# Kernel tuning notes

Hardware: AMD Instinct MI355X
Metric: run time of the kernel (lower is better)

The kernel has to match this reference:

```python
import jax, jax.numpy as jnp
import numpy as np

B, T, C, H = 2, 2048, 1024, 16
HD = C // H          # head_dim = 64
HALF = HD // 2       # rope half dim = 32
ROPE_BASE = 10000.0


def _build_sin_cos(seq_len, half_dim, base=ROPE_BASE):
    # mirrors build_sin_cos: angles[t, i] = t * base^(-2i / (2*half_dim))
    pos = jnp.arange(seq_len, dtype=jnp.float32)[:, None]                     # [T,1]
    inv_freq = 1.0 / (base ** (jnp.arange(0, half_dim * 2, 2, dtype=jnp.float32) / (half_dim * 2)))
    angles = pos * inv_freq                                                   # [T, half]
    return jnp.sin(angles), jnp.cos(angles)


def setup_inputs() -> dict:
    key = jax.random.key(0)
    k1, k2, k3 = jax.random.split(key, 3)
    x = jax.random.normal(k1, (B, T, C), dtype=jnp.float32)
    # nn.Linear weights (stored as [out,in] in torch; we keep [in,out] for x @ W)
    Wqkv = jax.random.normal(k2, (C, 3 * C), dtype=jnp.float32) * (C ** -0.5)
    Wproj = jax.random.normal(k3, (C, C), dtype=jnp.float32) * (C ** -0.5)
    rope_sin, rope_cos = _build_sin_cos(T, HALF)
    return {"x": x, "Wqkv": Wqkv, "Wproj": Wproj, "rope_sin": rope_sin, "rope_cos": rope_cos}


def reference(x, Wqkv, Wproj, rope_sin, rope_cos):
    Bb, Tt, Cc = x.shape
    Hh = H
    hd = Cc // Hh
    # fused QKV projection, then per-head split (matches view(B,T,H,3*hd).split)
    qkv = (x @ Wqkv).reshape(Bb, Tt, Hh, 3 * hd)
    q, k, v = jnp.split(qkv, 3, axis=-1)                                      # each [B,T,H,hd]
    # RoPE (single device path: local slice == full range)
    s = rope_sin[:Tt][None, :, None, :].astype(x.dtype)                       # [1,T,1,half]
    c = rope_cos[:Tt][None, :, None, :].astype(x.dtype)

    def rot(t):
        t1, t2 = jnp.split(t, 2, axis=-1)
        return jnp.concatenate([t1 * c - t2 * s, t1 * s + t2 * c], axis=-1)

    q = rot(q)
    k = rot(k)
    # causal scaled dot-product attention (flash_attn default scale = hd^-0.5)
    scale = jnp.asarray(hd, x.dtype) ** -0.5
    scores = jnp.einsum('bqhd,bkhd->bhqk', q, k) * scale                      # [B,H,T,T]
    causal = jnp.tril(jnp.ones((Tt, Tt), dtype=bool))
    scores = jnp.where(causal, scores, jnp.finfo(x.dtype).min)
    probs = jax.nn.softmax(scores, axis=-1)
    attn = jnp.einsum('bhqk,bkhd->bqhd', probs, v).reshape(Bb, Tt, Cc)
    return attn @ Wproj
```

## Files before the change

### kernel.cpp

```cpp
#include <hip/hip_runtime.h>

#define Bb 2
#define Tt 2048
#define Cc_ 1024
#define Hh 16
#define HDd 64

typedef __attribute__((ext_vector_type(8))) short bf16x8;
typedef __attribute__((ext_vector_type(4))) float f32x4;
typedef __attribute__((ext_vector_type(4))) unsigned short u16x4;
typedef __attribute__((ext_vector_type(2))) unsigned int u32x2;

__device__ __forceinline__ unsigned short f2bf(float f) {
  union { float f; unsigned int u; } v; v.f = f;
  unsigned int r = v.u + 0x7FFFu + ((v.u >> 16) & 1u);
  return (unsigned short)(r >> 16);
}
__device__ __forceinline__ float bf2f(unsigned short u) {
  union { unsigned int u; float f; } v; v.u = ((unsigned int)u) << 16;
  return v.f;
}
__device__ __forceinline__ unsigned int cvtpk(float lo, float hi) {
  unsigned int r;
  asm("v_cvt_pk_bf16_f32 %0, %1, %2" : "=v"(r) : "v"(lo), "v"(hi));
  return r;
}
__device__ __forceinline__ f32x4 mfma16(bf16x8 a, bf16x8 b, f32x4 c) {
  return __builtin_amdgcn_mfma_f32_16x16x32_bf16(a, b, c, 0, 0, 0);
}
__device__ __forceinline__ void gl_lds16(const void* g, void* l) {
  auto* gp = reinterpret_cast<const __attribute__((address_space(1))) unsigned int*>(
      reinterpret_cast<unsigned long long>(g));
  auto* lp = reinterpret_cast<__attribute__((address_space(3))) unsigned int*>(
      reinterpret_cast<unsigned long long>(l));
  __builtin_amdgcn_global_load_lds(gp, lp, 16, 0, 0);
}

__global__ __launch_bounds__(256) void k_cvt(const float* __restrict__ in,
                                             unsigned short* __restrict__ out, int n4) {
  const int i = blockIdx.x * 256 + threadIdx.x;
  if (i >= n4) return;
  f32x4 v = ((const f32x4*)in)[i];
  u16x4 o;
  o[0] = f2bf(v[0]); o[1] = f2bf(v[1]); o[2] = f2bf(v[2]); o[3] = f2bf(v[3]);
  ((u16x4*)out)[i] = o;
}

__global__ __launch_bounds__(256) void k_tcvt(const float* __restrict__ in,
                                              unsigned short* __restrict__ out, int R, int Cc) {
  __shared__ float tile[32][33];
  const int c0 = blockIdx.x * 32, r0 = blockIdx.y * 32;
  const int tx = threadIdx.x, ty = threadIdx.y;
#pragma unroll
  for (int i = 0; i < 4; ++i)
    tile[ty + i * 8][tx] = in[(size_t)(r0 + ty + i * 8) * Cc + c0 + tx];
  __syncthreads();
#pragma unroll
  for (int i = 0; i < 4; ++i)
    out[(size_t)(c0 + ty + i * 8) * R + r0 + tx] = f2bf(tile[tx][ty + i * 8]);
}

template <bool OUT_BF16>
__global__ __launch_bounds__(256) void k_gemm(const unsigned short* __restrict__ A,
                                              const unsigned short* __restrict__ Bt,
                                              void* __restrict__ Cout, int M, int N, int K) {
  __shared__ unsigned short lA[128 * 64];
  __shared__ unsigned short lB[128 * 64];
  const int tid = threadIdx.x;
  const int lane = tid & 63, wid = tid >> 6;
  const int wr = wid >> 1, wc = wid & 1;
  const int bm = blockIdx.y * 128, bn = blockIdx.x * 128;
  const int l15 = lane & 15, l4 = lane >> 4;
  f32x4 acc[4][4];
#pragma unroll
  for (int i = 0; i < 4; ++i)
#pragma unroll
    for (int j = 0; j < 4; ++j) acc[i][j] = f32x4{0.f, 0.f, 0.f, 0.f};
  const int nk = K >> 6;
  for (int t = 0; t < nk; ++t) {
    const int k0 = t << 6;
    __syncthreads();
#pragma unroll
    for (int i = 0; i < 4; ++i) {
      const int slot = i * 256 + tid;
      const int row = slot >> 3, g = slot & 7;
      const int gs = (g ^ (row & 7)) * 8;
      gl_lds16(A + (size_t)(bm + row) * K + k0 + gs, &lA[slot * 8]);
      gl_lds16(Bt + (size_t)(bn + row) * K + k0 + gs, &lB[slot * 8]);
    }
    __syncthreads();
#pragma unroll
    for (int ks = 0; ks < 2; ++ks) {
      bf16x8 af[4], bfr[4];
#pragma unroll
      for (int mf = 0; mf < 4; ++mf) {
        const int row = wr * 64 + mf * 16 + l15;
        const int g = ks * 4 + l4;
        af[mf] = *(const bf16x8*)&lA[row * 64 + ((g ^ (row & 7)) * 8)];
      }
#pragma unroll
      for (int nf = 0; nf < 4; ++nf) {
        const int row = wc * 64 + nf * 16 + l15;
        const int g = ks * 4 + l4;
        bfr[nf] = *(const bf16x8*)&lB[row * 64 + ((g ^ (row & 7)) * 8)];
      }
#pragma unroll
      for (int mf = 0; mf < 4; ++mf)
#pragma unroll
        for (int nf = 0; nf < 4; ++nf)
          acc[mf][nf] = mfma16(af[mf], bfr[nf], acc[mf][nf]);
    }
  }
  const int rb = bm + wr * 64 + l4 * 4;
  const int cb = bn + wc * 64 + l15;
#pragma unroll
  for (int mf = 0; mf < 4; ++mf)
#pragma unroll
    for (int nf = 0; nf < 4; ++nf)
#pragma unroll
      for (int j = 0; j < 4; ++j) {
        const size_t idx = (size_t)(rb + mf * 16 + j) * N + cb + nf * 16;
        if (OUT_BF16)
          ((unsigned short*)Cout)[idx] = f2bf(acc[mf][nf][j]);
        else
          ((float*)Cout)[idx] = acc[mf][nf][j];
      }
}

__global__ __launch_bounds__(256) void k_gemm64(const unsigned short* __restrict__ A,
                                                const unsigned short* __restrict__ Bt,
                                                float* __restrict__ Cout, int M, int N, int K) {
  __shared__ unsigned short lA[128 * 64];
  __shared__ unsigned short lB[64 * 64];
  const int tid = threadIdx.x;
  const int lane = tid & 63, w = tid >> 6;
  const int bm = blockIdx.y * 128, bn = blockIdx.x * 64;
  const int l15 = lane & 15, l4 = lane >> 4;
  f32x4 acc[2][4];
#pragma unroll
  for (int i = 0; i < 2; ++i)
#pragma unroll
    for (int j = 0; j < 4; ++j) acc[i][j] = f32x4{0.f, 0.f, 0.f, 0.f};
  const int nk = K >> 6;
  for (int t = 0; t < nk; ++t) {
    const int k0 = t << 6;
    __syncthreads();
#pragma unroll
    for (int i = 0; i < 4; ++i) {
      const int slot = i * 256 + tid;
      const int row = slot >> 3, g = slot & 7;
      const int gs = (g ^ (row & 7)) * 8;
      gl_lds16(A + (size_t)(bm + row) * K + k0 + gs, &lA[slot * 8]);
    }
#pragma unroll
    for (int i = 0; i < 2; ++i) {
      const int slot = i * 256 + tid;
      const int row = slot >> 3, g = slot & 7;
      const int gs = (g ^ (row & 7)) * 8;
      gl_lds16(Bt + (size_t)(bn + row) * K + k0 + gs, &lB[slot * 8]);
    }
    __syncthreads();
#pragma unroll
    for (int ks = 0; ks < 2; ++ks) {
      bf16x8 af[2], bfr[4];
#pragma unroll
      for (int mf = 0; mf < 2; ++mf) {
        const int row = w * 32 + mf * 16 + l15;
        const int g = ks * 4 + l4;
        af[mf] = *(const bf16x8*)&lA[row * 64 + ((g ^ (row & 7)) * 8)];
      }
#pragma unroll
      for (int nf = 0; nf < 4; ++nf) {
        const int row = nf * 16 + l15;
        const int g = ks * 4 + l4;
        bfr[nf] = *(const bf16x8*)&lB[row * 64 + ((g ^ (row & 7)) * 8)];
      }
#pragma unroll
      for (int mf = 0; mf < 2; ++mf)
#pragma unroll
        for (int nf = 0; nf < 4; ++nf)
          acc[mf][nf] = mfma16(af[mf], bfr[nf], acc[mf][nf]);
    }
  }
  const int rb = bm + w * 32 + l4 * 4;
  const int cb = bn + l15;
#pragma unroll
  for (int mf = 0; mf < 2; ++mf)
#pragma unroll
    for (int nf = 0; nf < 4; ++nf)
#pragma unroll
      for (int j = 0; j < 4; ++j)
        Cout[(size_t)(rb + mf * 16 + j) * N + cb + nf * 16] = acc[mf][nf][j];
}

__global__ __launch_bounds__(256) void k_rope(const unsigned short* __restrict__ qkv,
                                              const float* __restrict__ rsin,
                                              const float* __restrict__ rcos,
                                              unsigned short* __restrict__ Q,
                                              unsigned short* __restrict__ K) {
  const int tid = blockIdx.x * 256 + threadIdx.x;
  const int d = tid & 31;
  const int t = (tid >> 5) & 2047;
  const int h = (tid >> 16) & 15;
  const int b = tid >> 20;
  const size_t rq = (size_t)(b * Tt + t) * 3072 + h * 192;
  const float q1 = bf2f(qkv[rq + d]), q2 = bf2f(qkv[rq + 32 + d]);
  const float k1 = bf2f(qkv[rq + 64 + d]), k2 = bf2f(qkv[rq + 96 + d]);
  const float s = rsin[t * 32 + d], c = rcos[t * 32 + d];
  const size_t ob = ((size_t)(b * Hh + h) * Tt + t) * 64 + d;
  const float qs = 0.125f * 1.44269504088896f;
  Q[ob] = f2bf((q1 * c - q2 * s) * qs);
  Q[ob + 32] = f2bf((q1 * s + q2 * c) * qs);
  K[ob] = f2bf(k1 * c - k2 * s);
  K[ob + 32] = f2bf(k1 * s + k2 * c);
}

__global__ __launch_bounds__(256) void k_vrep(const unsigned short* __restrict__ qkv,
                                              unsigned short* __restrict__ Vt) {
  __shared__ unsigned short tile[32][72];
  const int bh = blockIdx.y;
  const int t0 = blockIdx.x * 32;
  const int tx = threadIdx.x, ty = threadIdx.y;
  const int b = bh >> 4, h = bh & 15;
#pragma unroll
  for (int i = 0; i < 4; ++i) {
    const int trow = ty + i * 8;
    const size_t r = (size_t)(b * Tt + t0 + trow) * 3072 + h * 192 + 128;
    tile[trow][tx] = qkv[r + tx];
    tile[trow][tx + 32] = qkv[r + 32 + tx];
  }
  __syncthreads();
#pragma unroll
  for (int i = 0; i < 8; ++i) {
    const int d = ty + i * 8;
    Vt[((size_t)bh * 64 + d) * Tt + t0 + tx] = tile[tx][d];
  }
}

__global__ __launch_bounds__(256, 4) void k_attn(const unsigned short* __restrict__ Q,
                                                 const unsigned short* __restrict__ Kt,
                                                 const unsigned short* __restrict__ Vt,
                                                 unsigned short* __restrict__ Aout) {
  __shared__ unsigned short lK[2 * 64 * 64];
  __shared__ unsigned short lV[2 * 64 * 64];
  __shared__ unsigned short lP[4 * 16 * 64];
  const int bid = blockIdx.x;
  const int xcd = bid & 7, ss = bid >> 3;
  const int cc = ss & 31, kk = ss >> 5;
  const int bh = xcd * 4 + kk;
  const int c2 = (cc + ((kk & 2) ? 16 : 0)) & 31;
  const int qt = (kk & 1) ? (31 - c2) : c2;
  const int b = bh >> 4, h = bh & 15;
  const int tid = threadIdx.x, lane = tid & 63, w = tid >> 6;
  const int l15 = lane & 15, l4 = lane >> 4;
  const int qb = qt * 64;
  const unsigned short* Kbh = Kt + (size_t)bh * Tt * 64;
  const unsigned short* Vbh = Vt + (size_t)bh * 64 * Tt;

  int fo[4][2];
#pragma unroll
  for (int a = 0; a < 4; ++a)
#pragma unroll
    for (int bb = 0; bb < 2; ++bb)
      fo[a][bb] = ((a * 16 + l15) * 64 + (((bb * 4 + l4) ^ (l15 & 7)) * 8)) * 2;
  int pwo[4];
#pragma unroll
  for (int nf = 0; nf < 4; ++nf)
    pwo[nf] = (l15 * 64 + (((nf * 2 + (l4 >> 1)) ^ (l15 & 7)) * 8) + (l4 & 1) * 4) * 2;
  char* const pB = (char*)lP + w * 2048;
  char* const kB0 = (char*)lK;
  char* const vB0 = (char*)lV;
  const int rA = tid >> 3;
  const int gsA = ((tid & 7) ^ (rA & 7)) * 8;
  const int kgA = rA * 64 + gsA;
  const int vgA = rA * 2048 + gsA;
  char* const ldKA = (char*)lK + tid * 16;
  char* const ldVA = (char*)lV + tid * 16;

#define STAGE(BUF, TT)                                                   \
  {                                                                      \
    const int kv_ = (TT) * 64;                                           \
    gl_lds16(Kbh + kv_ * 64 + kgA, ldKA + (BUF) * 8192);                 \
    gl_lds16(Kbh + kv_ * 64 + kgA + 32 * 64, ldKA + (BUF) * 8192 + 4096);\
    gl_lds16(Vbh + kv_ + vgA, ldVA + (BUF) * 8192);                      \
    gl_lds16(Vbh + kv_ + vgA + 32 * 2048, ldVA + (BUF) * 8192 + 4096);   \
  }

  const size_t qoff = ((size_t)bh * Tt + qb + w * 16 + l15) * 64 + l4 * 8;
  const bf16x8 qf0 = *(const bf16x8*)&Q[qoff];
  const bf16x8 qf1 = *(const bf16x8*)&Q[qoff + 32];
  f32x4 o[4];
#pragma unroll
  for (int i = 0; i < 4; ++i) o[i] = f32x4{0.f, 0.f, 0.f, 0.f};
  float mrun = -1e30f, lrun = 0.f;
  const int nt = qt + 1;

#define BODY(CUR, T, LASTT)                                                       \
  {                                                                               \
    if ((T) + 1 < nt) STAGE(CUR ^ 1, (T) + 1);                                    \
    f32x4 sv[4];                                                                  \
    _Pragma("unroll") for (int i = 0; i < 4; ++i) sv[i] = f32x4{0.f, 0.f, 0.f, 0.f}; \
    __builtin_amdgcn_s_setprio(1);                                                \
    _Pragma("unroll") for (int ks = 0; ks < 2; ++ks) {                            \
      const bf16x8 qa = ks ? qf1 : qf0;                                           \
      _Pragma("unroll") for (int nf = 0; nf < 4; ++nf) {                          \
        const bf16x8 kf = *(const bf16x8*)(kB0 + (CUR) * 8192 + fo[nf][ks]);      \
        sv[nf] = mfma16(kf, qa, sv[nf]);                                          \
      }                                                                           \
    }                                                                             \
    __builtin_amdgcn_s_setprio(0);                                                \
    if (LASTT) {                                                                  \
      _Pragma("unroll") for (int nf = 0; nf < 4; ++nf)                            \
        _Pragma("unroll") for (int j = 0; j < 4; ++j)                             \
          if (nf * 16 + l4 * 4 + j > w * 16 + l15) sv[nf][j] = -3e38f;            \
    }                                                                             \
    float mx = fmaxf(fmaxf(fmaxf(sv[0][0], sv[0][1]), fmaxf(sv[0][2], sv[0][3])), \
                     fmaxf(fmaxf(sv[1][0], sv[1][1]), fmaxf(sv[1][2], sv[1][3])));\
    mx = fmaxf(mx, fmaxf(fmaxf(fmaxf(sv[2][0], sv[2][1]), fmaxf(sv[2][2], sv[2][3])), \
                         fmaxf(fmaxf(sv[3][0], sv[3][1]), fmaxf(sv[3][2], sv[3][3])))); \
    if (!__all(mx - mrun <= 8.0f)) {                                              \
      mx = fmaxf(mx, __shfl_xor(mx, 16, 64));                                     \
      mx = fmaxf(mx, __shfl_xor(mx, 32, 64));                                     \
      const float mnew = fmaxf(mrun, mx);                                         \
      const float alpha = exp2f(mrun - mnew);                                     \
      lrun *= alpha;                                                              \
      float aj[4];                                                                \
      _Pragma("unroll") for (int j = 0; j < 4; ++j) aj[j] = __shfl(alpha, l4 * 4 + j, 64); \
      _Pragma("unroll") for (int df = 0; df < 4; ++df)                            \
        _Pragma("unroll") for (int j = 0; j < 4; ++j) o[df][j] *= aj[j];          \
      mrun = mnew;                                                                \
    }                                                                             \
    _Pragma("unroll") for (int nf = 0; nf < 4; ++nf) {                            \
      const float p0 = exp2f(sv[nf][0] - mrun), p1 = exp2f(sv[nf][1] - mrun);     \
      const float p2 = exp2f(sv[nf][2] - mrun), p3 = exp2f(sv[nf][3] - mrun);     \
      lrun += (p0 + p1) + (p2 + p3);                                              \
      u32x2 pk; pk[0] = cvtpk(p0, p1); pk[1] = cvtpk(p2, p3);                     \
      *(u32x2*)(pB + pwo[nf]) = pk;                                               \
    }                                                                             \
    __builtin_amdgcn_s_setprio(1);                                                \
    _Pragma("unroll") for (int kb = 0; kb < 2; ++kb) {                            \
      const bf16x8 pa = *(const bf16x8*)(pB + fo[0][kb]);                         \
      _Pragma("unroll") for (int df = 0; df < 4; ++df) {                          \
        const bf16x8 vb = *(const bf16x8*)(vB0 + (CUR) * 8192 + fo[df][kb]);      \
        o[df] = mfma16(pa, vb, o[df]);                                            \
      }                                                                           \
    }                                                                             \
    __builtin_amdgcn_s_setprio(0);                                                \
    if ((T) + 1 < nt) asm volatile("s_waitcnt vmcnt(0)" ::: "memory");            \
    __builtin_amdgcn_s_barrier();                                                 \
  }

  STAGE(0, 0);
  asm volatile("s_waitcnt vmcnt(0)" ::: "memory");
  __builtin_amdgcn_s_barrier();
  int t = 0;
  for (; t + 2 < nt; t += 2) {
    BODY(0, t, false);
    BODY(1, t + 1, false);
  }
  if (nt - t == 2) {
    BODY(0, t, false);
    BODY(1, t + 1, true);
  } else {
    BODY(0, t, true);
  }
#undef BODY
#undef STAGE

  lrun += __shfl_xor(lrun, 16, 64);
  lrun += __shfl_xor(lrun, 32, 64);
  const float rinv = 1.f / lrun;
  float lj[4];
#pragma unroll
  for (int j = 0; j < 4; ++j) lj[j] = __shfl(rinv, l4 * 4 + j, 64);
#pragma unroll
  for (int j = 0; j < 4; ++j) {
    const size_t rr = (size_t)(b * Tt + qb + w * 16 + l4 * 4 + j) * 1024 + h * 64 + l15;
#pragma unroll
    for (int df = 0; df < 4; ++df) Aout[rr + df * 16] = f2bf(o[df][j] * lj[j]);
  }
}

extern "C" void kernel_launch(void* const* d_in, const int* in_sizes, int n_in,
                              void* d_out, int out_size, void* d_ws, size_t ws_size,
                              hipStream_t stream) {
  const float* x = (const float*)d_in[0];
  const float* Wqkv = (const float*)d_in[1];
  const float* Wproj = (const float*)d_in[2];
  const float* rsin = (const float*)d_in[3];
  const float* rcos = (const float*)d_in[4];
  float* out = (float*)d_out;
  char* ws = (char*)d_ws;
  unsigned short* xb = (unsigned short*)(ws);
  unsigned short* wqkvt = (unsigned short*)(ws + (size_t)(8 << 20));
  unsigned short* wprot = (unsigned short*)(ws + (size_t)(14 << 20));
  unsigned short* qkv = (unsigned short*)(ws + (size_t)(16 << 20));
  unsigned short* Q = (unsigned short*)(ws + (size_t)(40 << 20));
  unsigned short* K = (unsigned short*)(ws + (size_t)(48 << 20));
  unsigned short* Vt = (unsigned short*)(ws + (size_t)(56 << 20));
  unsigned short* attn = (unsigned short*)(ws + (size_t)(64 << 20));

  k_cvt<<<4096, 256, 0, stream>>>(x, xb, 1048576);
  k_tcvt<<<dim3(96, 32), dim3(32, 8), 0, stream>>>(Wqkv, wqkvt, 1024, 3072);
  k_tcvt<<<dim3(32, 32), dim3(32, 8), 0, stream>>>(Wproj, wprot, 1024, 1024);
  k_gemm<true><<<dim3(24, 32), 256, 0, stream>>>(xb, wqkvt, qkv, 4096, 3072, 1024);
  k_rope<<<8192, 256, 0, stream>>>(qkv, rsin, rcos, Q, K);
  k_vrep<<<dim3(64, 32), dim3(32, 8), 0, stream>>>(qkv, Vt);
  k_attn<<<1024, 256, 0, stream>>>(Q, K, Vt, attn);
  k_gemm64<<<dim3(16, 32), 256, 0, stream>>>(attn, wprot, out, 4096, 1024, 1024);
}
```

Baseline: 194.9 us.

## Fuse RoPE into QKV GEMM epilogue, merge prep kernels, double-buffer output GEMM

The three conversion and transpose kernels are merged into one launch. The Wqkv columns are permuted so each 128-wide GEMM tile holds contiguous Q, K or V head data, which lets RoPE and the Q scale run in the QKV GEMM epilogue and write Q and K directly. This removes the full bf16 qkv round trip and the separate rope kernel; only V goes through a temporary buffer. The output projection GEMM gains double-buffered LDS prefetch with one barrier per step and priority hints, at the cost of more LDS per block.

```diff
diff --git a/kernel.cpp b/kernel.cpp
--- a/kernel.cpp
+++ b/kernel.cpp
@@ -36,36 +36,59 @@
   __builtin_amdgcn_global_load_lds(gp, lp, 16, 0, 0);
 }
 
-__global__ __launch_bounds__(256) void k_cvt(const float* __restrict__ in,
-                                             unsigned short* __restrict__ out, int n4) {
-  const int i = blockIdx.x * 256 + threadIdx.x;
-  if (i >= n4) return;
-  f32x4 v = ((const f32x4*)in)[i];
-  u16x4 o;
-  o[0] = f2bf(v[0]); o[1] = f2bf(v[1]); o[2] = f2bf(v[2]); o[3] = f2bf(v[3]);
-  ((u16x4*)out)[i] = o;
-}
-
-__global__ __launch_bounds__(256) void k_tcvt(const float* __restrict__ in,
-                                              unsigned short* __restrict__ out, int R, int Cc) {
+__global__ __launch_bounds__(256) void k_prep(const float* __restrict__ x,
+                                              const float* __restrict__ Wqkv,
+                                              const float* __restrict__ Wproj,
+                                              unsigned short* __restrict__ xb,
+                                              unsigned short* __restrict__ wqkvt,
+                                              unsigned short* __restrict__ wprot) {
+  const int bid = blockIdx.x;
+  const int tid = threadIdx.x;
+  if (bid < 4096) {
+    const int i = bid * 256 + tid;
+    f32x4 v = ((const f32x4*)x)[i];
+    u16x4 o;
+    o[0] = f2bf(v[0]); o[1] = f2bf(v[1]); o[2] = f2bf(v[2]); o[3] = f2bf(v[3]);
+    ((u16x4*)xb)[i] = o;
+    return;
+  }
   __shared__ float tile[32][33];
-  const int c0 = blockIdx.x * 32, r0 = blockIdx.y * 32;
-  const int tx = threadIdx.x, ty = threadIdx.y;
+  const int tx = tid & 31, ty = tid >> 5;
+  if (bid < 4096 + 3072) {
+    const int tt = bid - 4096;
+    const int n0 = (tt % 96) * 32, k0 = (tt / 96) * 32;
+    const int region = n0 >> 10, nl = n0 & 1023;
+    const int ob = (nl >> 6) * 192 + region * 64 + (nl & 63);
+#pragma unroll
+    for (int i = 0; i < 4; ++i)
+      tile[ty + i * 8][tx] = Wqkv[(size_t)(k0 + ty + i * 8) * 3072 + ob + tx];
+    __syncthreads();
+#pragma unroll
+    for (int i = 0; i < 4; ++i)
+      wqkvt[(size_t)(n0 + ty + i * 8) * 1024 + k0 + tx] = f2bf(tile[tx][ty + i * 8]);
+    return;
+  }
+  const int tt = bid - 7168;
+  const int c0 = (tt & 31) * 32, r0 = (tt >> 5) * 32;
 #pragma unroll
   for (int i = 0; i < 4; ++i)
-    tile[ty + i * 8][tx] = in[(size_t)(r0 + ty + i * 8) * Cc + c0 + tx];
+    tile[ty + i * 8][tx] = Wproj[(size_t)(r0 + ty + i * 8) * 1024 + c0 + tx];
   __syncthreads();
 #pragma unroll
   for (int i = 0; i < 4; ++i)
-    out[(size_t)(c0 + ty + i * 8) * R + r0 + tx] = f2bf(tile[tx][ty + i * 8]);
-}
-
-template <bool OUT_BF16>
-__global__ __launch_bounds__(256) void k_gemm(const unsigned short* __restrict__ A,
-                                              const unsigned short* __restrict__ Bt,
-                                              void* __restrict__ Cout, int M, int N, int K) {
+    wprot[(size_t)(c0 + ty + i * 8) * 1024 + r0 + tx] = f2bf(tile[tx][ty + i * 8]);
+}
+
+__global__ __launch_bounds__(256) void k_gemm_qkv(const unsigned short* __restrict__ A,
+                                                  const unsigned short* __restrict__ Bt,
+                                                  const float* __restrict__ rsin,
+                                                  const float* __restrict__ rcos,
+                                                  unsigned short* __restrict__ Qo,
+                                                  unsigned short* __restrict__ Ko,
+                                                  unsigned short* __restrict__ vtmp) {
   __shared__ unsigned short lA[128 * 64];
   __shared__ unsigned short lB[128 * 64];
+  const int K = 1024;
   const int tid = threadIdx.x;
   const int lane = tid & 63, wid = tid >> 6;
   const int wr = wid >> 1, wc = wid & 1;
@@ -76,8 +99,7 @@
   for (int i = 0; i < 4; ++i)
 #pragma unroll
     for (int j = 0; j < 4; ++j) acc[i][j] = f32x4{0.f, 0.f, 0.f, 0.f};
-  const int nk = K >> 6;
-  for (int t = 0; t < nk; ++t) {
+  for (int t = 0; t < 16; ++t) {
     const int k0 = t << 6;
     __syncthreads();
 #pragma unroll
@@ -112,110 +134,41 @@
     }
   }
   const int rb = bm + wr * 64 + l4 * 4;
-  const int cb = bn + wc * 64 + l15;
-#pragma unroll
-  for (int mf = 0; mf < 4; ++mf)
-#pragma unroll
-    for (int nf = 0; nf < 4; ++nf)
+  const int region = blockIdx.x >> 3;
+  if (region < 2) {
+    const int h = (blockIdx.x & 7) * 2 + wc;
+    unsigned short* dst = (region == 0) ? Qo : Ko;
+    const float qs = (region == 0) ? (0.125f * 1.44269504088896f) : 1.0f;
+#pragma unroll
+    for (int mf = 0; mf < 4; ++mf)
 #pragma unroll
       for (int j = 0; j < 4; ++j) {
-        const size_t idx = (size_t)(rb + mf * 16 + j) * N + cb + nf * 16;
-        if (OUT_BF16)
-          ((unsigned short*)Cout)[idx] = f2bf(acc[mf][nf][j]);
-        else
-          ((float*)Cout)[idx] = acc[mf][nf][j];
+        const int trow = rb + mf * 16 + j;
+        const int bi = trow >> 11, t = trow & 2047;
+        const size_t rowb = ((size_t)(bi * Hh + h) * Tt + t) * 64;
+#pragma unroll
+        for (int nf = 0; nf < 2; ++nf) {
+          const int d = nf * 16 + l15;
+          const float sn = rsin[t * 32 + d], cs = rcos[t * 32 + d];
+          const float a1 = acc[mf][nf][j], a2 = acc[mf][nf + 2][j];
+          dst[rowb + d] = f2bf((a1 * cs - a2 * sn) * qs);
+          dst[rowb + d + 32] = f2bf((a1 * sn + a2 * cs) * qs);
+        }
       }
-}
-
-__global__ __launch_bounds__(256) void k_gemm64(const unsigned short* __restrict__ A,
-                                                const unsigned short* __restrict__ Bt,
-                                                float* __restrict__ Cout, int M, int N, int K) {
-  __shared__ unsigned short lA[128 * 64];
-  __shared__ unsigned short lB[64 * 64];
-  const int tid = threadIdx.x;
-  const int lane = tid & 63, w = tid >> 6;
-  const int bm = blockIdx.y * 128, bn = blockIdx.x * 64;
-  const int l15 = lane & 15, l4 = lane >> 4;
-  f32x4 acc[2][4];
-#pragma unroll
-  for (int i = 0; i < 2; ++i)
-#pragma unroll
-    for (int j = 0; j < 4; ++j) acc[i][j] = f32x4{0.f, 0.f, 0.f, 0.f};
-  const int nk = K >> 6;
-  for (int t = 0; t < nk; ++t) {
-    const int k0 = t << 6;
-    __syncthreads();
-#pragma unroll
-    for (int i = 0; i < 4; ++i) {
-      const int slot = i * 256 + tid;
-      const int row = slot >> 3, g = slot & 7;
-      const int gs = (g ^ (row & 7)) * 8;
-      gl_lds16(A + (size_t)(bm + row) * K + k0 + gs, &lA[slot * 8]);
-    }
-#pragma unroll
-    for (int i = 0; i < 2; ++i) {
-      const int slot = i * 256 + tid;
-      const int row = slot >> 3, g = slot & 7;
-      const int gs = (g ^ (row & 7)) * 8;
-      gl_lds16(Bt + (size_t)(bn + row) * K + k0 + gs, &lB[slot * 8]);
-    }
-    __syncthreads();
-#pragma unroll
-    for (int ks = 0; ks < 2; ++ks) {
-      bf16x8 af[2], bfr[4];
-#pragma unroll
-      for (int mf = 0; mf < 2; ++mf) {
-        const int row = w * 32 + mf * 16 + l15;
-        const int g = ks * 4 + l4;
-        af[mf] = *(const bf16x8*)&lA[row * 64 + ((g ^ (row & 7)) * 8)];
-      }
-#pragma unroll
-      for (int nf = 0; nf < 4; ++nf) {
-        const int row = nf * 16 + l15;
-        const int g = ks * 4 + l4;
-        bfr[nf] = *(const bf16x8*)&lB[row * 64 + ((g ^ (row & 7)) * 8)];
-      }
-#pragma unroll
-      for (int mf = 0; mf < 2; ++mf)
-#pragma unroll
-        for (int nf = 0; nf < 4; ++nf)
-          acc[mf][nf] = mfma16(af[mf], bfr[nf], acc[mf][nf]);
-    }
-  }
-  const int rb = bm + w * 32 + l4 * 4;
-  const int cb = bn + l15;
-#pragma unroll
-  for (int mf = 0; mf < 2; ++mf)
-#pragma unroll
-    for (int nf = 0; nf < 4; ++nf)
-#pragma unroll
-      for (int j = 0; j < 4; ++j)
-        Cout[(size_t)(rb + mf * 16 + j) * N + cb + nf * 16] = acc[mf][nf][j];
-}
-
-__global__ __launch_bounds__(256) void k_rope(const unsigned short* __restrict__ qkv,
-                                              const float* __restrict__ rsin,
-                                              const float* __restrict__ rcos,
-                                              unsigned short* __restrict__ Q,
-                                              unsigned short* __restrict__ K) {
-  const int tid = blockIdx.x * 256 + threadIdx.x;
-  const int d = tid & 31;
-  const int t = (tid >> 5) & 2047;
-  const int h = (tid >> 16) & 15;
-  const int b = tid >> 20;
-  const size_t rq = (size_t)(b * Tt + t) * 3072 + h * 192;
-  const float q1 = bf2f(qkv[rq + d]), q2 = bf2f(qkv[rq + 32 + d]);
-  const float k1 = bf2f(qkv[rq + 64 + d]), k2 = bf2f(qkv[rq + 96 + d]);
-  const float s = rsin[t * 32 + d], c = rcos[t * 32 + d];
-  const size_t ob = ((size_t)(b * Hh + h) * Tt + t) * 64 + d;
-  const float qs = 0.125f * 1.44269504088896f;
-  Q[ob] = f2bf((q1 * c - q2 * s) * qs);
-  Q[ob + 32] = f2bf((q1 * s + q2 * c) * qs);
-  K[ob] = f2bf(k1 * c - k2 * s);
-  K[ob + 32] = f2bf(k1 * s + k2 * c);
-}
-
-__global__ __launch_bounds__(256) void k_vrep(const unsigned short* __restrict__ qkv,
+  } else {
+    const int colb = (blockIdx.x & 7) * 128 + wc * 64;
+#pragma unroll
+    for (int mf = 0; mf < 4; ++mf)
+#pragma unroll
+      for (int nf = 0; nf < 4; ++nf)
+#pragma unroll
+        for (int j = 0; j < 4; ++j)
+          vtmp[(size_t)(rb + mf * 16 + j) * 1024 + colb + nf * 16 + l15] =
+              f2bf(acc[mf][nf][j]);
+  }
+}
+
+__global__ __launch_bounds__(256) void k_vrep(const unsigned short* __restrict__ vtmp,
                                               unsigned short* __restrict__ Vt) {
   __shared__ unsigned short tile[32][72];
   const int bh = blockIdx.y;
@@ -225,9 +178,9 @@
 #pragma unroll
   for (int i = 0; i < 4; ++i) {
     const int trow = ty + i * 8;
-    const size_t r = (size_t)(b * Tt + t0 + trow) * 3072 + h * 192 + 128;
-    tile[trow][tx] = qkv[r + tx];
-    tile[trow][tx + 32] = qkv[r + 32 + tx];
+    const size_t r = (size_t)(b * Tt + t0 + trow) * 1024 + h * 64;
+    tile[trow][tx] = vtmp[r + tx];
+    tile[trow][tx + 32] = vtmp[r + 32 + tx];
   }
   __syncthreads();
 #pragma unroll
@@ -381,6 +334,83 @@
   }
 }
 
+__global__ __launch_bounds__(256) void k_gemm2(const unsigned short* __restrict__ A,
+                                               const unsigned short* __restrict__ Bt,
+                                               float* __restrict__ Cout) {
+  __shared__ unsigned short lA[2][128 * 64];
+  __shared__ unsigned short lB[2][64 * 64];
+  const int K = 1024, N = 1024;
+  const int tid = threadIdx.x;
+  const int lane = tid & 63, w = tid >> 6;
+  const int bm = blockIdx.y * 128, bn = blockIdx.x * 64;
+  const int l15 = lane & 15, l4 = lane >> 4;
+  f32x4 acc[2][4];
+#pragma unroll
+  for (int i = 0; i < 2; ++i)
+#pragma unroll
+    for (int j = 0; j < 4; ++j) acc[i][j] = f32x4{0.f, 0.f, 0.f, 0.f};
+
+#define STG(BUF, TT)                                                        \
+  {                                                                         \
+    const int k0 = (TT) << 6;                                               \
+    _Pragma("unroll") for (int i = 0; i < 4; ++i) {                         \
+      const int slot = i * 256 + tid;                                       \
+      const int row = slot >> 3, g = slot & 7;                              \
+      const int gs = (g ^ (row & 7)) * 8;                                   \
+      gl_lds16(A + (size_t)(bm + row) * K + k0 + gs, &lA[BUF][slot * 8]);   \
+    }                                                                       \
+    _Pragma("unroll") for (int i = 0; i < 2; ++i) {                         \
+      const int slot = i * 256 + tid;                                       \
+      const int row = slot >> 3, g = slot & 7;                              \
+      const int gs = (g ^ (row & 7)) * 8;                                   \
+      gl_lds16(Bt + (size_t)(bn + row) * K + k0 + gs, &lB[BUF][slot * 8]);  \
+    }                                                                       \
+  }
+
+  STG(0, 0);
+  asm volatile("s_waitcnt vmcnt(0)" ::: "memory");
+  __builtin_amdgcn_s_barrier();
+  for (int t = 0; t < 16; ++t) {
+    const int cur = t & 1;
+    if (t + 1 < 16) STG(cur ^ 1, t + 1);
+    __builtin_amdgcn_s_setprio(1);
+#pragma unroll
+    for (int ks = 0; ks < 2; ++ks) {
+      bf16x8 af[2], bfr[4];
+#pragma unroll
+      for (int mf = 0; mf < 2; ++mf) {
+        const int row = w * 32 + mf * 16 + l15;
+        const int g = ks * 4 + l4;
+        af[mf] = *(const bf16x8*)&lA[cur][row * 64 + ((g ^ (row & 7)) * 8)];
+      }
+#pragma unroll
+      for (int nf = 0; nf < 4; ++nf) {
+        const int row = nf * 16 + l15;
+        const int g = ks * 4 + l4;
+        bfr[nf] = *(const bf16x8*)&lB[cur][row * 64 + ((g ^ (row & 7)) * 8)];
+      }
+#pragma unroll
+      for (int mf = 0; mf < 2; ++mf)
+#pragma unroll
+        for (int nf = 0; nf < 4; ++nf)
+          acc[mf][nf] = mfma16(af[mf], bfr[nf], acc[mf][nf]);
+    }
+    __builtin_amdgcn_s_setprio(0);
+    if (t + 1 < 16) asm volatile("s_waitcnt vmcnt(0)" ::: "memory");
+    __builtin_amdgcn_s_barrier();
+  }
+#undef STG
+  const int rb = bm + w * 32 + l4 * 4;
+  const int cb = bn + l15;
+#pragma unroll
+  for (int mf = 0; mf < 2; ++mf)
+#pragma unroll
+    for (int nf = 0; nf < 4; ++nf)
+#pragma unroll
+      for (int j = 0; j < 4; ++j)
+        Cout[(size_t)(rb + mf * 16 + j) * N + cb + nf * 16] = acc[mf][nf][j];
+}
+
 extern "C" void kernel_launch(void* const* d_in, const int* in_sizes, int n_in,
                               void* d_out, int out_size, void* d_ws, size_t ws_size,
                               hipStream_t stream) {
@@ -394,18 +424,15 @@
   unsigned short* xb = (unsigned short*)(ws);
   unsigned short* wqkvt = (unsigned short*)(ws + (size_t)(8 << 20));
   unsigned short* wprot = (unsigned short*)(ws + (size_t)(14 << 20));
-  unsigned short* qkv = (unsigned short*)(ws + (size_t)(16 << 20));
+  unsigned short* vtmp = (unsigned short*)(ws + (size_t)(16 << 20));
   unsigned short* Q = (unsigned short*)(ws + (size_t)(40 << 20));
   unsigned short* K = (unsigned short*)(ws + (size_t)(48 << 20));
   unsigned short* Vt = (unsigned short*)(ws + (size_t)(56 << 20));
   unsigned short* attn = (unsigned short*)(ws + (size_t)(64 << 20));
 
-  k_cvt<<<4096, 256, 0, stream>>>(x, xb, 1048576);
-  k_tcvt<<<dim3(96, 32), dim3(32, 8), 0, stream>>>(Wqkv, wqkvt, 1024, 3072);
-  k_tcvt<<<dim3(32, 32), dim3(32, 8), 0, stream>>>(Wproj, wprot, 1024, 1024);
-  k_gemm<true><<<dim3(24, 32), 256, 0, stream>>>(xb, wqkvt, qkv, 4096, 3072, 1024);
-  k_rope<<<8192, 256, 0, stream>>>(qkv, rsin, rcos, Q, K);
-  k_vrep<<<dim3(64, 32), dim3(32, 8), 0, stream>>>(qkv, Vt);
+  k_prep<<<8192, 256, 0, stream>>>(x, Wqkv, Wproj, xb, wqkvt, wprot);
+  k_gemm_qkv<<<dim3(24, 32), 256, 0, stream>>>(xb, wqkvt, rsin, rcos, Q, K, vtmp);
+  k_vrep<<<dim3(64, 32), dim3(32, 8), 0, stream>>>(vtmp, Vt);
   k_attn<<<1024, 256, 0, stream>>>(Q, K, Vt, attn);
-  k_gemm64<<<dim3(16, 32), 256, 0, stream>>>(attn, wprot, out, 4096, 1024, 1024);
-}
+  k_gemm2<<<dim3(16, 32), 256, 0, stream>>>(attn, wprot, out);
+}
```

Result: faster. 186.3 us (-4.4%).
